# Performance work log

Hardware: AMD Instinct MI355X
Metric: run time of the kernel (lower is better)

The kernel has to match this reference:

```python
import jax, jax.numpy as jnp
import numpy as np

# Model constants (from TinyRecursiveModel defaults)
IN = 200        # input feature dim (hard-coded Linear(200, d_model))
D = 64          # d_model
NH = 2          # nhead (head_dim = 32); with seq_len=1 attention is trivial
FF = 64         # dim_feedforward
LAYERS = 2      # TransformerEncoder num_layers
STEPS = 16      # recursion_steps
B = 65536       # batch size
EPS = 1e-5      # torch LayerNorm eps


def setup_inputs() -> dict:
    key = jax.random.key(0)
    ks = jax.random.split(key, 14)
    w = lambda k, shape, s=0.05: (jax.random.normal(k, shape, jnp.float32) * s)
    return {
        "x": jax.random.normal(ks[0], (B, IN), jnp.float32),
        # input_proj: Linear(200, 64)
        "input_w": w(ks[1], (D, IN)), "input_b": w(ks[2], (D,)),
        # per-layer MHA: packed in_proj (q,k,v) and out_proj, stacked over LAYERS
        "Wqkv": w(ks[3], (LAYERS, 3 * D, D)), "bqkv": w(ks[4], (LAYERS, 3 * D)),
        "Wo": w(ks[5], (LAYERS, D, D)), "bo": w(ks[6], (LAYERS, D)),
        "ln1_g": jnp.ones((LAYERS, D), jnp.float32), "ln1_b": jnp.zeros((LAYERS, D), jnp.float32),
        # per-layer FFN: Linear(64,64) -> relu -> Linear(64,64)
        "W1": w(ks[7], (LAYERS, FF, D)), "b1": w(ks[8], (LAYERS, FF)),
        "W2": w(ks[9], (LAYERS, D, FF)), "b2": w(ks[10], (LAYERS, D)),
        "ln2_g": jnp.ones((LAYERS, D), jnp.float32), "ln2_b": jnp.zeros((LAYERS, D), jnp.float32),
        # output_proj: Linear(64, 1)
        "out_w": w(ks[11], (1, D)), "out_b": w(ks[12], (1,)),
    }


def _ln(x, g, b):
    m = jnp.mean(x, axis=-1, keepdims=True)
    v = jnp.var(x, axis=-1, keepdims=True)
    return (x - m) * jax.lax.rsqrt(v + EPS) * g + b


def reference(x, input_w, input_b, Wqkv, bqkv, Wo, bo, ln1_g, ln1_b,
              W1, b1, W2, b2, ln2_g, ln2_b, out_w, out_b):
    h = x @ input_w.T + input_b  # [B, D]; seq dim of size 1 is kept implicit

    def layer(h, l):
        # seq_len == 1: softmax over a single key is identically 1, so the
        # attention output equals V exactly (Q/K have zero influence & zero grad).
        Wv = Wqkv[l, 2 * D:3 * D]
        bv = bqkv[l, 2 * D:3 * D]
        v = h @ Wv.T + bv                     # [B, D]
        sa = v @ Wo[l].T + bo[l]              # out_proj
        h = _ln(h + sa, ln1_g[l], ln1_b[l])   # post-norm (torch default)
        ff = jax.nn.relu(h @ W1[l].T + b1[l]) @ W2[l].T + b2[l]
        return _ln(h + ff, ln2_g[l], ln2_b[l])

    def step(h, _):
        for l in range(LAYERS):  # 2 structurally distinct layers
            h = layer(h, l)
        return h, None

    h, _ = jax.lax.scan(step, h, None, length=STEPS)
    out = h @ out_w.T + out_b  # [B, 1]
    return out[:, 0]           # squeeze -> [B]
```

## Files before the change

### kernel.cpp

```cpp
#include <hip/hip_runtime.h>


using f16x8 = __attribute__((ext_vector_type(8))) _Float16;
using f32x4 = __attribute__((ext_vector_type(4))) float;

#define DI __device__ __forceinline__

namespace {

constexpr int RS = 144;
constexpr float EPS = 1e-5f;

DI unsigned packh2(float a, float b) {
  _Float16 lo = (_Float16)a, hi = (_Float16)b;
  unsigned short ul = __builtin_bit_cast(unsigned short, lo);
  unsigned short uh = __builtin_bit_cast(unsigned short, hi);
  return ((unsigned)uh << 16) | (unsigned)ul;
}

DI f16x8 cvt8h(f32x4 a, f32x4 b) {
  f16x8 r;
  r[0] = (_Float16)a[0]; r[1] = (_Float16)a[1];
  r[2] = (_Float16)a[2]; r[3] = (_Float16)a[3];
  r[4] = (_Float16)b[0]; r[5] = (_Float16)b[1];
  r[6] = (_Float16)b[2]; r[7] = (_Float16)b[3];
  return r;
}

DI unsigned pkmax0(unsigned t) {
  unsigned r;
  asm("v_pk_max_f16 %0, %1, 0" : "=v"(r) : "v"(t));
  return r;
}

DI void swap16(unsigned& a, unsigned& b) {
#if __has_builtin(__builtin_amdgcn_permlane16_swap)
  auto r = __builtin_amdgcn_permlane16_swap(a, b, false, false);
  a = r[0]; b = r[1];
#else
  unsigned ax = (unsigned)__shfl_xor((int)a, 16);
  unsigned bx = (unsigned)__shfl_xor((int)b, 16);
  bool odd = (threadIdx.x & 16) != 0;
  unsigned na = odd ? bx : a;
  unsigned nb = odd ? b : ax;
  a = na; b = nb;
#endif
}
DI void swap32(unsigned& a, unsigned& b) {
#if __has_builtin(__builtin_amdgcn_permlane32_swap)
  auto r = __builtin_amdgcn_permlane32_swap(a, b, false, false);
  a = r[0]; b = r[1];
#else
  unsigned ax = (unsigned)__shfl_xor((int)a, 32);
  unsigned bx = (unsigned)__shfl_xor((int)b, 32);
  bool hi = (threadIdx.x & 32) != 0;
  unsigned na = hi ? bx : a;
  unsigned nb = hi ? b : ax;
  a = na; b = nb;
#endif
}

DI float reduce4(float x) {
  unsigned a = __builtin_bit_cast(unsigned, x), b = a;
  swap16(a, b);
  float x1 = __builtin_bit_cast(float, a) + __builtin_bit_cast(float, b);
  unsigned c = __builtin_bit_cast(unsigned, x1), d = c;
  swap32(c, d);
  return __builtin_bit_cast(float, c) + __builtin_bit_cast(float, d);
}

union BU {
  unsigned u[8];
  struct { f16x8 b0, b1; } f;
};

template <bool RELU>
DI void packacc(const f32x4 (&acc)[4], BU& o) {
#pragma unroll
  for (int tp = 0; tp < 4; ++tp) {
    unsigned p0 = packh2(acc[tp][0], acc[tp][1]);
    unsigned p1 = packh2(acc[tp][2], acc[tp][3]);
    if (RELU) { p0 = pkmax0(p0); p1 = pkmax0(p1); }
    o.u[2 * tp + 0] = p0;
    o.u[2 * tp + 1] = p1;
  }
}

DI void exchange(BU& o) {
  swap32(o.u[0], o.u[2]); swap32(o.u[1], o.u[3]);
  swap32(o.u[4], o.u[6]); swap32(o.u[5], o.u[7]);
  swap16(o.u[0], o.u[2]); swap16(o.u[1], o.u[3]);
  swap16(o.u[4], o.u[6]); swap16(o.u[5], o.u[7]);
}

struct WFrag { f16x8 f[4][2]; };

DI WFrag loadW(const float* W, int l15, int g) {
  WFrag w;
#pragma unroll
  for (int tp = 0; tp < 4; ++tp)
#pragma unroll
    for (int s = 0; s < 2; ++s) {
      const float* p = W + (16 * tp + l15) * 64 + 32 * s + 8 * g;
      w.f[tp][s] = cvt8h(*(const f32x4*)p, *(const f32x4*)(p + 4));
    }
  return w;
}

DI f32x4 mfma(f16x8 a, f16x8 b, f32x4 c) {
  return __builtin_amdgcn_mfma_f32_16x16x32_f16(a, b, c, 0, 0, 0);
}

DI void lnorm(const f32x4 (&a)[4], const float* gb, int g, f32x4 (&h)[4]) {
  float s = 0.f, q = 0.f;
#pragma unroll
  for (int tp = 0; tp < 4; ++tp)
#pragma unroll
    for (int r = 0; r < 4; ++r) { float x = a[tp][r]; s += x; q = fmaf(x, x, q); }
  s = reduce4(s); q = reduce4(q);
  float mean = s * 0.015625f;
  float var  = fmaf(q, 0.015625f, -mean * mean);
  float rs   = rsqrtf(var + EPS);
  float u    = -mean * rs;
  const f32x4* gv = (const f32x4*)gb;
#pragma unroll
  for (int tp = 0; tp < 4; ++tp) {
    f32x4 gg = gv[4 * tp + g];
    f32x4 bb = gv[16 + 4 * tp + g];
#pragma unroll
    for (int r = 0; r < 4; ++r)
      h[tp][r] = fmaf(fmaf(a[tp][r], rs, u), gg[r], bb[r]);
  }
}

struct alignas(16) Smem {
  char  mats[4][64 * RS];
  float params[2 * 7 * 64];
};

DI void do_layer(f32x4 (&hA)[4], f32x4 (&hB)[4], BU& bA, BU& bB,
                 const WFrag& wvo, const char* w1b, const char* w2b,
                 const float* prm, int g) {
  const f32x4* pv = (const f32x4*)prm;
  f32x4 aA[4], aB[4];
#pragma unroll
  for (int tp = 0; tp < 4; ++tp) {
    aA[tp] = mfma(wvo.f[tp][1], bA.f.b1, mfma(wvo.f[tp][0], bA.f.b0, hA[tp]));
    aB[tp] = mfma(wvo.f[tp][1], bB.f.b1, mfma(wvo.f[tp][0], bB.f.b0, hB[tp]));
    f32x4 bv = pv[4 * tp + g];
    aA[tp] += bv; aB[tp] += bv;
  }
  lnorm(aA, prm + 192, g, hA);
  lnorm(aB, prm + 192, g, hB);
  packacc<false>(hA, bA); packacc<false>(hB, bB);
  exchange(bA); exchange(bB);
#pragma unroll
  for (int tp = 0; tp < 4; ++tp) {
    f16x8 a0 = *(const f16x8*)(w1b + tp * 16 * RS);
    f16x8 a1 = *(const f16x8*)(w1b + tp * 16 * RS + 64);
    f32x4 cin = pv[16 + 4 * tp + g];
    aA[tp] = mfma(a1, bA.f.b1, mfma(a0, bA.f.b0, cin));
    aB[tp] = mfma(a1, bB.f.b1, mfma(a0, bB.f.b0, cin));
  }
  packacc<true>(aA, bA); packacc<true>(aB, bB);
  exchange(bA); exchange(bB);
#pragma unroll
  for (int tp = 0; tp < 4; ++tp) {
    f16x8 a0 = *(const f16x8*)(w2b + tp * 16 * RS);
    f16x8 a1 = *(const f16x8*)(w2b + tp * 16 * RS + 64);
    aA[tp] = mfma(a1, bA.f.b1, mfma(a0, bA.f.b0, hA[tp]));
    aB[tp] = mfma(a1, bB.f.b1, mfma(a0, bB.f.b0, hB[tp]));
    f32x4 bv = pv[32 + 4 * tp + g];
    aA[tp] += bv; aB[tp] += bv;
  }
  lnorm(aA, prm + 320, g, hA);
  lnorm(aB, prm + 320, g, hB);
  packacc<false>(hA, bA); packacc<false>(hB, bB);
  exchange(bA); exchange(bB);
}

__global__ __launch_bounds__(256) void precompute_kernel(
    const float* __restrict__ Wqkv, const float* __restrict__ bqkv,
    const float* __restrict__ Wo, const float* __restrict__ bo,
    float* __restrict__ ws) {
  __shared__ float wv[4096];
  __shared__ float wo[4096];
  const int l = blockIdx.x;
  const float* Wv  = Wqkv + l * (192 * 64) + 128 * 64;
  const float* WoL = Wo + l * 4096;
  for (int e = threadIdx.x; e < 4096; e += 256) { wv[e] = Wv[e]; wo[e] = WoL[e]; }
  __syncthreads();
  float* wvo = ws + l * 4096;
  const int i = threadIdx.x >> 2, j0 = (threadIdx.x & 3) * 16;
  float acc[16];
#pragma unroll
  for (int jj = 0; jj < 16; ++jj) acc[jj] = 0.f;
  for (int k = 0; k < 64; ++k) {
    float a = wo[i * 64 + k];
#pragma unroll
    for (int jj = 0; jj < 16; ++jj) acc[jj] = fmaf(a, wv[k * 64 + j0 + jj], acc[jj]);
  }
#pragma unroll
  for (int jj = 0; jj < 16; ++jj) wvo[i * 64 + j0 + jj] = acc[jj];
  if (threadIdx.x < 64) {
    const int i2 = threadIdx.x;
    const float* bv = bqkv + l * 192 + 128;
    float s = bo[l * 64 + i2];
    for (int k = 0; k < 64; ++k) s = fmaf(wo[i2 * 64 + k], bv[k], s);
    ws[2 * 4096 + l * 64 + i2] = s;
  }
}

__global__ __launch_bounds__(256, 2) void trm5_kernel(
    const float* __restrict__ x, const float* __restrict__ input_w,
    const float* __restrict__ input_b, const float* __restrict__ W1,
    const float* __restrict__ b1, const float* __restrict__ W2,
    const float* __restrict__ b2, const float* __restrict__ ln1_g,
    const float* __restrict__ ln1_b, const float* __restrict__ ln2_g,
    const float* __restrict__ ln2_b, const float* __restrict__ out_w,
    const float* __restrict__ out_b, const float* __restrict__ ws,
    float* __restrict__ out) {
  __shared__ Smem sm;
  const int tid = threadIdx.x;
  const int w = tid >> 6, lane = tid & 63;
  const int l15 = lane & 15, g = lane >> 4;
  const int row0 = blockIdx.x * 128 + w * 32;

  {
    const float* srcs[4] = {W1, W1 + 4096, W2, W2 + 4096};
#pragma unroll
    for (int m = 0; m < 4; ++m) {
      char* dst = sm.mats[m];
      const float* src = srcs[m];
      for (int e = tid; e < 512; e += 256) {
        int row = e >> 3, c8 = (e & 7) * 8;
        const float* p = src + row * 64 + c8;
        *(f16x8*)(dst + row * RS + 2 * c8) =
            cvt8h(*(const f32x4*)p, *(const f32x4*)(p + 4));
      }
    }
  }
  for (int e = tid; e < 896; e += 256) {
    int l = e / 448, r = e % 448, v = r >> 6, j = r & 63;
    const float* src;
    switch (v) {
      case 0:  src = ws + 2 * 4096 + l * 64; break;
      case 1:  src = b1 + l * 64; break;
      case 2:  src = b2 + l * 64; break;
      case 3:  src = ln1_g + l * 64; break;
      case 4:  src = ln1_b + l * 64; break;
      case 5:  src = ln2_g + l * 64; break;
      default: src = ln2_b + l * 64; break;
    }
    sm.params[l * 448 + v * 64 + j] = src[j];
  }

  WFrag wvo0 = loadW(ws, l15, g);
  WFrag wvo1 = loadW(ws + 4096, l15, g);

  const char* w1b0 = sm.mats[0] + l15 * RS + 16 * g;
  const char* w1b1 = sm.mats[1] + l15 * RS + 16 * g;
  const char* w2b0 = sm.mats[2] + l15 * RS + 16 * g;
  const char* w2b1 = sm.mats[3] + l15 * RS + 16 * g;

  f32x4 hA[4], hB[4];
#pragma unroll
  for (int tp = 0; tp < 4; ++tp) {
    f32x4 ib = *(const f32x4*)(input_b + 16 * tp + 4 * g);
    hA[tp] = ib; hB[tp] = ib;
  }
  {
    const float* xA = x + (size_t)(row0 + l15) * 200;
    const float* xB = xA + 16 * 200;
    const f32x4 zero = {0.f, 0.f, 0.f, 0.f};
    for (int s7 = 0; s7 < 7; ++s7) {
      int kb = 32 * s7 + 8 * g;
      bool v0 = kb < 200;
      f32x4 xa0 = v0 ? *(const f32x4*)(xA + kb) : zero;
      f32x4 xa1 = v0 ? *(const f32x4*)(xA + kb + 4) : zero;
      f32x4 xb0 = v0 ? *(const f32x4*)(xB + kb) : zero;
      f32x4 xb1 = v0 ? *(const f32x4*)(xB + kb + 4) : zero;
      f16x8 bfA = cvt8h(xa0, xa1);
      f16x8 bfB = cvt8h(xb0, xb1);
#pragma unroll
      for (int tp = 0; tp < 4; ++tp) {
        const float* wr = input_w + (16 * tp + l15) * 200;
        f32x4 wa = v0 ? *(const f32x4*)(wr + kb) : zero;
        f32x4 wb = v0 ? *(const f32x4*)(wr + kb + 4) : zero;
        f16x8 af = cvt8h(wa, wb);
        hA[tp] = mfma(af, bfA, hA[tp]);
        hB[tp] = mfma(af, bfB, hB[tp]);
      }
    }
  }
  BU bA, bB;
  packacc<false>(hA, bA); packacc<false>(hB, bB);
  exchange(bA); exchange(bB);
  __syncthreads();

#pragma unroll 1
  for (int step = 0; step < 16; ++step) {
    do_layer(hA, hB, bA, bB, wvo0, w1b0, w2b0, sm.params,       g);
    do_layer(hA, hB, bA, bB, wvo1, w1b1, w2b1, sm.params + 448, g);
  }

  float pA = 0.f, pB = 0.f;
#pragma unroll
  for (int tp = 0; tp < 4; ++tp) {
    f32x4 ow = *(const f32x4*)(out_w + 16 * tp + 4 * g);
#pragma unroll
    for (int r = 0; r < 4; ++r) {
      pA = fmaf(hA[tp][r], ow[r], pA);
      pB = fmaf(hB[tp][r], ow[r], pB);
    }
  }
  pA += __shfl_xor(pA, 16); pA += __shfl_xor(pA, 32);
  pB += __shfl_xor(pB, 16); pB += __shfl_xor(pB, 32);
  if (lane < 16) {
    float ob = out_b[0];
    out[row0 + l15]      = pA + ob;
    out[row0 + 16 + l15] = pB + ob;
  }
}

}

extern "C" void kernel_launch(void* const* d_in, const int* in_sizes, int n_in,
                              void* d_out, int out_size, void* d_ws, size_t ws_size,
                              hipStream_t stream) {
  const float* x       = (const float*)d_in[0];
  const float* input_w = (const float*)d_in[1];
  const float* input_b = (const float*)d_in[2];
  const float* Wqkv    = (const float*)d_in[3];
  const float* bqkv    = (const float*)d_in[4];
  const float* Wo      = (const float*)d_in[5];
  const float* bo      = (const float*)d_in[6];
  const float* ln1_g   = (const float*)d_in[7];
  const float* ln1_b   = (const float*)d_in[8];
  const float* W1      = (const float*)d_in[9];
  const float* b1      = (const float*)d_in[10];
  const float* W2      = (const float*)d_in[11];
  const float* b2      = (const float*)d_in[12];
  const float* ln2_g   = (const float*)d_in[13];
  const float* ln2_b   = (const float*)d_in[14];
  const float* out_w   = (const float*)d_in[15];
  const float* out_b   = (const float*)d_in[16];
  float* out = (float*)d_out;
  float* ws  = (float*)d_ws;

  hipLaunchKernelGGL(precompute_kernel, dim3(2), dim3(256), 0, stream,
                     Wqkv, bqkv, Wo, bo, ws);
  hipLaunchKernelGGL(trm5_kernel, dim3(512), dim3(256), 0, stream,
                     x, input_w, input_b, W1, b1, W2, b2, ln1_g, ln1_b,
                     ln2_g, ln2_b, out_w, out_b, ws, out);
}
```

Measured before the change: 117.3 us.

## Process one 16-row tile per wave instead of two and raise occupancy

Each wave now carries a single 16-row tile through the recursive layers instead of two interleaved tiles, which halves register use per thread. Launch bounds go from 2 to 4 blocks per CU, and the grid doubles to 1024 blocks of 64 rows each. The aim is to hide MFMA, LDS-exchange and layernorm latency with more resident waves rather than with instruction-level parallelism inside each wave. In exchange, the per-block weight staging into shared memory is repeated by twice as many blocks, and each wave loses the overlap it used to get from two independent chains.

Result: slower. 242.9 us (+107.0%).

```diff
diff --git a/kernel.cpp b/kernel.cpp
--- a/kernel.cpp
+++ b/kernel.cpp
@@ -138,45 +138,36 @@
   float params[2 * 7 * 64];
 };
 
-DI void do_layer(f32x4 (&hA)[4], f32x4 (&hB)[4], BU& bA, BU& bB,
-                 const WFrag& wvo, const char* w1b, const char* w2b,
-                 const float* prm, int g) {
+DI void do_layer(f32x4 (&h)[4], BU& b, const WFrag& wvo, const char* w1b,
+                 const char* w2b, const float* prm, int g) {
   const f32x4* pv = (const f32x4*)prm;
-  f32x4 aA[4], aB[4];
-#pragma unroll
-  for (int tp = 0; tp < 4; ++tp) {
-    aA[tp] = mfma(wvo.f[tp][1], bA.f.b1, mfma(wvo.f[tp][0], bA.f.b0, hA[tp]));
-    aB[tp] = mfma(wvo.f[tp][1], bB.f.b1, mfma(wvo.f[tp][0], bB.f.b0, hB[tp]));
-    f32x4 bv = pv[4 * tp + g];
-    aA[tp] += bv; aB[tp] += bv;
-  }
-  lnorm(aA, prm + 192, g, hA);
-  lnorm(aB, prm + 192, g, hB);
-  packacc<false>(hA, bA); packacc<false>(hB, bB);
-  exchange(bA); exchange(bB);
+  f32x4 a[4];
+#pragma unroll
+  for (int tp = 0; tp < 4; ++tp) {
+    a[tp] = mfma(wvo.f[tp][1], b.f.b1, mfma(wvo.f[tp][0], b.f.b0, h[tp]));
+    a[tp] += pv[4 * tp + g];
+  }
+  lnorm(a, prm + 192, g, h);
+  packacc<false>(h, b);
+  exchange(b);
 #pragma unroll
   for (int tp = 0; tp < 4; ++tp) {
     f16x8 a0 = *(const f16x8*)(w1b + tp * 16 * RS);
     f16x8 a1 = *(const f16x8*)(w1b + tp * 16 * RS + 64);
-    f32x4 cin = pv[16 + 4 * tp + g];
-    aA[tp] = mfma(a1, bA.f.b1, mfma(a0, bA.f.b0, cin));
-    aB[tp] = mfma(a1, bB.f.b1, mfma(a0, bB.f.b0, cin));
-  }
-  packacc<true>(aA, bA); packacc<true>(aB, bB);
-  exchange(bA); exchange(bB);
+    a[tp] = mfma(a1, b.f.b1, mfma(a0, b.f.b0, pv[16 + 4 * tp + g]));
+  }
+  packacc<true>(a, b);
+  exchange(b);
 #pragma unroll
   for (int tp = 0; tp < 4; ++tp) {
     f16x8 a0 = *(const f16x8*)(w2b + tp * 16 * RS);
     f16x8 a1 = *(const f16x8*)(w2b + tp * 16 * RS + 64);
-    aA[tp] = mfma(a1, bA.f.b1, mfma(a0, bA.f.b0, hA[tp]));
-    aB[tp] = mfma(a1, bB.f.b1, mfma(a0, bB.f.b0, hB[tp]));
-    f32x4 bv = pv[32 + 4 * tp + g];
-    aA[tp] += bv; aB[tp] += bv;
-  }
-  lnorm(aA, prm + 320, g, hA);
-  lnorm(aB, prm + 320, g, hB);
-  packacc<false>(hA, bA); packacc<false>(hB, bB);
-  exchange(bA); exchange(bB);
+    a[tp] = mfma(a1, b.f.b1, mfma(a0, b.f.b0, h[tp]));
+    a[tp] += pv[32 + 4 * tp + g];
+  }
+  lnorm(a, prm + 320, g, h);
+  packacc<false>(h, b);
+  exchange(b);
 }
 
 __global__ __launch_bounds__(256) void precompute_kernel(
@@ -211,7 +202,7 @@
   }
 }
 
-__global__ __launch_bounds__(256, 2) void trm5_kernel(
+__global__ __launch_bounds__(256, 4) void trm6_kernel(
     const float* __restrict__ x, const float* __restrict__ input_w,
     const float* __restrict__ input_b, const float* __restrict__ W1,
     const float* __restrict__ b1, const float* __restrict__ W2,
@@ -224,7 +215,7 @@
   const int tid = threadIdx.x;
   const int w = tid >> 6, lane = tid & 63;
   const int l15 = lane & 15, g = lane >> 4;
-  const int row0 = blockIdx.x * 128 + w * 32;
+  const int row0 = blockIdx.x * 64 + w * 16;
 
   {
     const float* srcs[4] = {W1, W1 + 4096, W2, W2 + 4096};
@@ -263,64 +254,49 @@
   const char* w2b0 = sm.mats[2] + l15 * RS + 16 * g;
   const char* w2b1 = sm.mats[3] + l15 * RS + 16 * g;
 
-  f32x4 hA[4], hB[4];
-#pragma unroll
-  for (int tp = 0; tp < 4; ++tp) {
-    f32x4 ib = *(const f32x4*)(input_b + 16 * tp + 4 * g);
-    hA[tp] = ib; hB[tp] = ib;
-  }
+  f32x4 h[4];
+#pragma unroll
+  for (int tp = 0; tp < 4; ++tp)
+    h[tp] = *(const f32x4*)(input_b + 16 * tp + 4 * g);
   {
-    const float* xA = x + (size_t)(row0 + l15) * 200;
-    const float* xB = xA + 16 * 200;
+    const float* xr = x + (size_t)(row0 + l15) * 200;
     const f32x4 zero = {0.f, 0.f, 0.f, 0.f};
     for (int s7 = 0; s7 < 7; ++s7) {
       int kb = 32 * s7 + 8 * g;
       bool v0 = kb < 200;
-      f32x4 xa0 = v0 ? *(const f32x4*)(xA + kb) : zero;
-      f32x4 xa1 = v0 ? *(const f32x4*)(xA + kb + 4) : zero;
-      f32x4 xb0 = v0 ? *(const f32x4*)(xB + kb) : zero;
-      f32x4 xb1 = v0 ? *(const f32x4*)(xB + kb + 4) : zero;
-      f16x8 bfA = cvt8h(xa0, xa1);
-      f16x8 bfB = cvt8h(xb0, xb1);
+      f32x4 xa0 = v0 ? *(const f32x4*)(xr + kb) : zero;
+      f32x4 xa1 = v0 ? *(const f32x4*)(xr + kb + 4) : zero;
+      f16x8 bf = cvt8h(xa0, xa1);
 #pragma unroll
       for (int tp = 0; tp < 4; ++tp) {
         const float* wr = input_w + (16 * tp + l15) * 200;
         f32x4 wa = v0 ? *(const f32x4*)(wr + kb) : zero;
         f32x4 wb = v0 ? *(const f32x4*)(wr + kb + 4) : zero;
-        f16x8 af = cvt8h(wa, wb);
-        hA[tp] = mfma(af, bfA, hA[tp]);
-        hB[tp] = mfma(af, bfB, hB[tp]);
+        h[tp] = mfma(cvt8h(wa, wb), bf, h[tp]);
       }
     }
   }
-  BU bA, bB;
-  packacc<false>(hA, bA); packacc<false>(hB, bB);
-  exchange(bA); exchange(bB);
+  BU b;
+  packacc<false>(h, b);
+  exchange(b);
   __syncthreads();
 
 #pragma unroll 1
   for (int step = 0; step < 16; ++step) {
-    do_layer(hA, hB, bA, bB, wvo0, w1b0, w2b0, sm.params,       g);
-    do_layer(hA, hB, bA, bB, wvo1, w1b1, w2b1, sm.params + 448, g);
-  }
-
-  float pA = 0.f, pB = 0.f;
+    do_layer(h, b, wvo0, w1b0, w2b0, sm.params,       g);
+    do_layer(h, b, wvo1, w1b1, w2b1, sm.params + 448, g);
+  }
+
+  float p = 0.f;
 #pragma unroll
   for (int tp = 0; tp < 4; ++tp) {
     f32x4 ow = *(const f32x4*)(out_w + 16 * tp + 4 * g);
 #pragma unroll
-    for (int r = 0; r < 4; ++r) {
-      pA = fmaf(hA[tp][r], ow[r], pA);
-      pB = fmaf(hB[tp][r], ow[r], pB);
-    }
-  }
-  pA += __shfl_xor(pA, 16); pA += __shfl_xor(pA, 32);
-  pB += __shfl_xor(pB, 16); pB += __shfl_xor(pB, 32);
-  if (lane < 16) {
-    float ob = out_b[0];
-    out[row0 + l15]      = pA + ob;
-    out[row0 + 16 + l15] = pB + ob;
-  }
+    for (int r = 0; r < 4; ++r) p = fmaf(h[tp][r], ow[r], p);
+  }
+  p += __shfl_xor(p, 16);
+  p += __shfl_xor(p, 32);
+  if (lane < 16) out[row0 + l15] = p + out_b[0];
 }
 
 }
@@ -350,7 +326,7 @@
 
   hipLaunchKernelGGL(precompute_kernel, dim3(2), dim3(256), 0, stream,
                      Wqkv, bqkv, Wo, bo, ws);
-  hipLaunchKernelGGL(trm5_kernel, dim3(512), dim3(256), 0, stream,
+  hipLaunchKernelGGL(trm6_kernel, dim3(1024), dim3(256), 0, stream,
                      x, input_w, input_b, W1, b1, W2, b2, ln1_g, ln1_b,
                      ln2_g, ln2_b, out_w, out_b, ws, out);
 }
```

## Permute weight K-layout to drop lane exchanges; pack params in workspace

Applied to the files above, without the earlier changes.

Weight fragments (Wvo, W1, W2) are loaded with a permuted K ordering so that the MFMA accumulator layout can feed the next MFMA's B operand directly, which removes the per-layer swap-based exchange shuffles. Float-to-half packing uses the packed round-toward-zero conversion instead of two separate converts. Bias and LayerNorm parameters are gathered by the precompute kernel into the global workspace and read from there, no longer staged into shared memory. The two LayerNorms per stage are interleaved so their reductions can overlap. Round-toward-zero conversion slightly changes numerics, and parameter reads now go through global memory/cache rather than LDS.

New measurement: 108.2 us. -7.8%, faster.

```diff
diff --git a/kernel.cpp b/kernel.cpp
--- a/kernel.cpp
+++ b/kernel.cpp
@@ -2,6 +2,7 @@
 
 
 using f16x8 = __attribute__((ext_vector_type(8))) _Float16;
+using f16x2 = __attribute__((ext_vector_type(2))) _Float16;
 using f32x4 = __attribute__((ext_vector_type(4))) float;
 
 #define DI __device__ __forceinline__
@@ -11,11 +12,14 @@
 constexpr int RS = 144;
 constexpr float EPS = 1e-5f;
 
-DI unsigned packh2(float a, float b) {
-  _Float16 lo = (_Float16)a, hi = (_Float16)b;
-  unsigned short ul = __builtin_bit_cast(unsigned short, lo);
-  unsigned short uh = __builtin_bit_cast(unsigned short, hi);
-  return ((unsigned)uh << 16) | (unsigned)ul;
+DI unsigned pkrtz(float a, float b) {
+#if __has_builtin(__builtin_amdgcn_cvt_pkrtz)
+  return __builtin_bit_cast(unsigned, __builtin_amdgcn_cvt_pkrtz(a, b));
+#else
+  unsigned r;
+  asm("v_cvt_pkrtz_f16_f32 %0, %1, %2" : "=v"(r) : "v"(a), "v"(b));
+  return r;
+#endif
 }
 
 DI f16x8 cvt8h(f32x4 a, f32x4 b) {
@@ -78,21 +82,14 @@
 DI void packacc(const f32x4 (&acc)[4], BU& o) {
 #pragma unroll
   for (int tp = 0; tp < 4; ++tp) {
-    unsigned p0 = packh2(acc[tp][0], acc[tp][1]);
-    unsigned p1 = packh2(acc[tp][2], acc[tp][3]);
+    unsigned p0 = pkrtz(acc[tp][0], acc[tp][1]);
+    unsigned p1 = pkrtz(acc[tp][2], acc[tp][3]);
     if (RELU) { p0 = pkmax0(p0); p1 = pkmax0(p1); }
     o.u[2 * tp + 0] = p0;
     o.u[2 * tp + 1] = p1;
   }
 }
 
-DI void exchange(BU& o) {
-  swap32(o.u[0], o.u[2]); swap32(o.u[1], o.u[3]);
-  swap32(o.u[4], o.u[6]); swap32(o.u[5], o.u[7]);
-  swap16(o.u[0], o.u[2]); swap16(o.u[1], o.u[3]);
-  swap16(o.u[4], o.u[6]); swap16(o.u[5], o.u[7]);
-}
-
 struct WFrag { f16x8 f[4][2]; };
 
 DI WFrag loadW(const float* W, int l15, int g) {
@@ -101,8 +98,8 @@
   for (int tp = 0; tp < 4; ++tp)
 #pragma unroll
     for (int s = 0; s < 2; ++s) {
-      const float* p = W + (16 * tp + l15) * 64 + 32 * s + 8 * g;
-      w.f[tp][s] = cvt8h(*(const f32x4*)p, *(const f32x4*)(p + 4));
+      const float* p = W + (16 * tp + l15) * 64 + 32 * s + 4 * g;
+      w.f[tp][s] = cvt8h(*(const f32x4*)p, *(const f32x4*)(p + 16));
     }
   return w;
 }
@@ -111,36 +108,43 @@
   return __builtin_amdgcn_mfma_f32_16x16x32_f16(a, b, c, 0, 0, 0);
 }
 
-DI void lnorm(const f32x4 (&a)[4], const float* gb, int g, f32x4 (&h)[4]) {
-  float s = 0.f, q = 0.f;
+DI void lnorm2(const f32x4 (&aA)[4], const f32x4 (&aB)[4], const float* gb,
+               int g, f32x4 (&hA)[4], f32x4 (&hB)[4]) {
+  float sA = 0.f, qA = 0.f, sB = 0.f, qB = 0.f;
 #pragma unroll
   for (int tp = 0; tp < 4; ++tp)
 #pragma unroll
-    for (int r = 0; r < 4; ++r) { float x = a[tp][r]; s += x; q = fmaf(x, x, q); }
-  s = reduce4(s); q = reduce4(q);
-  float mean = s * 0.015625f;
-  float var  = fmaf(q, 0.015625f, -mean * mean);
-  float rs   = rsqrtf(var + EPS);
-  float u    = -mean * rs;
+    for (int r = 0; r < 4; ++r) {
+      float xa = aA[tp][r]; sA += xa; qA = fmaf(xa, xa, qA);
+      float xb = aB[tp][r]; sB += xb; qB = fmaf(xb, xb, qB);
+    }
+  sA = reduce4(sA); qA = reduce4(qA);
+  sB = reduce4(sB); qB = reduce4(qB);
+  float mA = sA * 0.015625f, mB = sB * 0.015625f;
+  float rA = rsqrtf(fmaf(qA, 0.015625f, -mA * mA) + EPS);
+  float rB = rsqrtf(fmaf(qB, 0.015625f, -mB * mB) + EPS);
+  float uA = -mA * rA, uB = -mB * rB;
   const f32x4* gv = (const f32x4*)gb;
 #pragma unroll
   for (int tp = 0; tp < 4; ++tp) {
     f32x4 gg = gv[4 * tp + g];
     f32x4 bb = gv[16 + 4 * tp + g];
 #pragma unroll
-    for (int r = 0; r < 4; ++r)
-      h[tp][r] = fmaf(fmaf(a[tp][r], rs, u), gg[r], bb[r]);
+    for (int r = 0; r < 4; ++r) {
+      hA[tp][r] = fmaf(fmaf(aA[tp][r], rA, uA), gg[r], bb[r]);
+      hB[tp][r] = fmaf(fmaf(aB[tp][r], rB, uB), gg[r], bb[r]);
+    }
   }
 }
 
 struct alignas(16) Smem {
-  char  mats[4][64 * RS];
-  float params[2 * 7 * 64];
+  char mats[4][64 * RS];
 };
 
 DI void do_layer(f32x4 (&hA)[4], f32x4 (&hB)[4], BU& bA, BU& bB,
                  const WFrag& wvo, const char* w1b, const char* w2b,
                  const float* prm, int g) {
+  asm("" : "+r"(prm));
   const f32x4* pv = (const f32x4*)prm;
   f32x4 aA[4], aB[4];
 #pragma unroll
@@ -150,10 +154,8 @@
     f32x4 bv = pv[4 * tp + g];
     aA[tp] += bv; aB[tp] += bv;
   }
-  lnorm(aA, prm + 192, g, hA);
-  lnorm(aB, prm + 192, g, hB);
+  lnorm2(aA, aB, prm + 192, g, hA, hB);
   packacc<false>(hA, bA); packacc<false>(hB, bB);
-  exchange(bA); exchange(bB);
 #pragma unroll
   for (int tp = 0; tp < 4; ++tp) {
     f16x8 a0 = *(const f16x8*)(w1b + tp * 16 * RS);
@@ -163,7 +165,6 @@
     aB[tp] = mfma(a1, bB.f.b1, mfma(a0, bB.f.b0, cin));
   }
   packacc<true>(aA, bA); packacc<true>(aB, bB);
-  exchange(bA); exchange(bB);
 #pragma unroll
   for (int tp = 0; tp < 4; ++tp) {
     f16x8 a0 = *(const f16x8*)(w2b + tp * 16 * RS);
@@ -173,15 +174,16 @@
     f32x4 bv = pv[32 + 4 * tp + g];
     aA[tp] += bv; aB[tp] += bv;
   }
-  lnorm(aA, prm + 320, g, hA);
-  lnorm(aB, prm + 320, g, hB);
+  lnorm2(aA, aB, prm + 320, g, hA, hB);
   packacc<false>(hA, bA); packacc<false>(hB, bB);
-  exchange(bA); exchange(bB);
 }
 
 __global__ __launch_bounds__(256) void precompute_kernel(
     const float* __restrict__ Wqkv, const float* __restrict__ bqkv,
     const float* __restrict__ Wo, const float* __restrict__ bo,
+    const float* __restrict__ b1, const float* __restrict__ b2,
+    const float* __restrict__ ln1_g, const float* __restrict__ ln1_b,
+    const float* __restrict__ ln2_g, const float* __restrict__ ln2_b,
     float* __restrict__ ws) {
   __shared__ float wv[4096];
   __shared__ float wo[4096];
@@ -202,22 +204,26 @@
   }
 #pragma unroll
   for (int jj = 0; jj < 16; ++jj) wvo[i * 64 + j0 + jj] = acc[jj];
+  float* prm = ws + 2 * 4096 + l * 448;
   if (threadIdx.x < 64) {
     const int i2 = threadIdx.x;
     const float* bv = bqkv + l * 192 + 128;
     float s = bo[l * 64 + i2];
     for (int k = 0; k < 64; ++k) s = fmaf(wo[i2 * 64 + k], bv[k], s);
-    ws[2 * 4096 + l * 64 + i2] = s;
-  }
-}
-
-__global__ __launch_bounds__(256, 2) void trm5_kernel(
+    prm[i2]       = s;
+    prm[64 + i2]  = b1[l * 64 + i2];
+    prm[128 + i2] = b2[l * 64 + i2];
+    prm[192 + i2] = ln1_g[l * 64 + i2];
+    prm[256 + i2] = ln1_b[l * 64 + i2];
+    prm[320 + i2] = ln2_g[l * 64 + i2];
+    prm[384 + i2] = ln2_b[l * 64 + i2];
+  }
+}
+
+__global__ __launch_bounds__(256, 2) void trm8_kernel(
     const float* __restrict__ x, const float* __restrict__ input_w,
     const float* __restrict__ input_b, const float* __restrict__ W1,
-    const float* __restrict__ b1, const float* __restrict__ W2,
-    const float* __restrict__ b2, const float* __restrict__ ln1_g,
-    const float* __restrict__ ln1_b, const float* __restrict__ ln2_g,
-    const float* __restrict__ ln2_b, const float* __restrict__ out_w,
+    const float* __restrict__ W2, const float* __restrict__ out_w,
     const float* __restrict__ out_b, const float* __restrict__ ws,
     float* __restrict__ out) {
   __shared__ Smem sm;
@@ -233,26 +239,12 @@
       char* dst = sm.mats[m];
       const float* src = srcs[m];
       for (int e = tid; e < 512; e += 256) {
-        int row = e >> 3, c8 = (e & 7) * 8;
-        const float* p = src + row * 64 + c8;
-        *(f16x8*)(dst + row * RS + 2 * c8) =
-            cvt8h(*(const f32x4*)p, *(const f32x4*)(p + 4));
+        int row = e >> 3, q = e & 7, s = q >> 2, gq = q & 3;
+        const float* p = src + row * 64 + 32 * s + 4 * gq;
+        *(f16x8*)(dst + row * RS + 64 * s + 16 * gq) =
+            cvt8h(*(const f32x4*)p, *(const f32x4*)(p + 16));
       }
     }
-  }
-  for (int e = tid; e < 896; e += 256) {
-    int l = e / 448, r = e % 448, v = r >> 6, j = r & 63;
-    const float* src;
-    switch (v) {
-      case 0:  src = ws + 2 * 4096 + l * 64; break;
-      case 1:  src = b1 + l * 64; break;
-      case 2:  src = b2 + l * 64; break;
-      case 3:  src = ln1_g + l * 64; break;
-      case 4:  src = ln1_b + l * 64; break;
-      case 5:  src = ln2_g + l * 64; break;
-      default: src = ln2_b + l * 64; break;
-    }
-    sm.params[l * 448 + v * 64 + j] = src[j];
   }
 
   WFrag wvo0 = loadW(ws, l15, g);
@@ -262,6 +254,8 @@
   const char* w1b1 = sm.mats[1] + l15 * RS + 16 * g;
   const char* w2b0 = sm.mats[2] + l15 * RS + 16 * g;
   const char* w2b1 = sm.mats[3] + l15 * RS + 16 * g;
+  const float* prm0 = ws + 2 * 4096;
+  const float* prm1 = ws + 2 * 4096 + 448;
 
   f32x4 hA[4], hB[4];
 #pragma unroll
@@ -295,13 +289,12 @@
   }
   BU bA, bB;
   packacc<false>(hA, bA); packacc<false>(hB, bB);
-  exchange(bA); exchange(bB);
   __syncthreads();
 
 #pragma unroll 1
   for (int step = 0; step < 16; ++step) {
-    do_layer(hA, hB, bA, bB, wvo0, w1b0, w2b0, sm.params,       g);
-    do_layer(hA, hB, bA, bB, wvo1, w1b1, w2b1, sm.params + 448, g);
+    do_layer(hA, hB, bA, bB, wvo0, w1b0, w2b0, prm0, g);
+    do_layer(hA, hB, bA, bB, wvo1, w1b1, w2b1, prm1, g);
   }
 
   float pA = 0.f, pB = 0.f;
@@ -349,8 +342,7 @@
   float* ws  = (float*)d_ws;
 
   hipLaunchKernelGGL(precompute_kernel, dim3(2), dim3(256), 0, stream,
-                     Wqkv, bqkv, Wo, bo, ws);
-  hipLaunchKernelGGL(trm5_kernel, dim3(512), dim3(256), 0, stream,
-                     x, input_w, input_b, W1, b1, W2, b2, ln1_g, ln1_b,
-                     ln2_g, ln2_b, out_w, out_b, ws, out);
-}
+                     Wqkv, bqkv, Wo, bo, b1, b2, ln1_g, ln1_b, ln2_g, ln2_b, ws);
+  hipLaunchKernelGGL(trm8_kernel, dim3(512), dim3(256), 0, stream,
+                     x, input_w, input_b, W1, W2, out_w, out_b, ws, out);
+}
```
